# Performance work log

Measured on AMD Instinct MI355X. Metric: run time of the kernel, lower is better.

Reference implementation:

```python
import jax, jax.numpy as jnp
import numpy as np
import math

B, N, D, SEQ = 4, 1024, 512, 256
HID, DIST_D, N_NER, N_LAB = 150, 128, 3, 4
SPANS_PER_WORD = 0.5
ASPECT, OPINION = 1, 2
NUM_DIST_EMB = 512


def setup_inputs() -> dict:
    key = jax.random.key(0)
    ks = jax.random.split(key, 9)
    starts = jax.random.randint(ks[0], (B, N), 0, SEQ)
    widths = jax.random.randint(ks[1], (B, N), 0, 8)
    ends = jnp.clip(starts + widths, 0, SEQ - 1)
    spans = jnp.stack([starts, ends], axis=-1).astype(jnp.int32)  # [B,N,2]
    ner_scores = jax.random.normal(ks[2], (B, N, N_NER), jnp.float32)
    span_embeddings = jax.random.normal(ks[3], (B, N, D), jnp.float32)
    span_mask = jnp.ones((B, N), dtype=bool)

    pair_dim = 2 * D + DIST_D

    def xavier(k, shape):
        std = math.sqrt(2.0 / (shape[0] + shape[1]))
        return jax.random.normal(k, shape, jnp.float32) * std

    dist_table = xavier(ks[4], (NUM_DIST_EMB, DIST_D))
    W1 = xavier(ks[5], (pair_dim, HID)); b1 = jnp.zeros((HID,), jnp.float32)
    W2 = xavier(ks[6], (HID, HID));      b2 = jnp.zeros((HID,), jnp.float32)
    Wc = xavier(ks[7], (HID, N_LAB));    bc = jnp.zeros((N_LAB,), jnp.float32)

    return dict(spans=spans, ner_scores=ner_scores, span_embeddings=span_embeddings,
                span_mask=span_mask, seq_length=SEQ, dist_table=dist_table,
                W1=W1, b1=b1, W2=W2, b2=b2, Wc=Wc, bc=bc)


def bucket_values(d, num_identity=4, num_total=10):
    # semi-logscale buckets: [0,1,2,3,4,5-7,8-15,16-31,32-63,64+]
    logspace = jnp.floor(jnp.log2(jnp.maximum(d, 1).astype(jnp.float32))).astype(jnp.int32) + (num_identity - 1)
    return jnp.clip(jnp.where(d <= num_identity, d, logspace), 0, num_total - 1)


def _prune(scores, mask, k):
    masked = jnp.where(mask, scores, jnp.float32(-1e20))
    _, idx = jax.lax.top_k(masked, k)  # [B,k]
    return idx


def reference(spans, ner_scores, span_embeddings, span_mask, seq_length,
              dist_table, W1, b1, W2, b2, Wc, bc):
    bsz, n_spans, d = span_embeddings.shape
    k = min(int(math.ceil(seq_length * SPANS_PER_WORD)), n_spans)

    a_idx = _prune(ner_scores[..., ASPECT], span_mask, k)    # [B,k]
    o_idx = _prune(ner_scores[..., OPINION], span_mask, k)
    a_keep = jnp.ones((bsz, k), dtype=bool)  # uniform seq_length -> all kept
    o_keep = a_keep

    gather = lambda t, i: jnp.take_along_axis(t, i[..., None], axis=1)
    a_emb = gather(span_embeddings, a_idx)   # [B,k,D]
    o_emb = gather(span_embeddings, o_idx)   # [B,k,D]
    spans_a = gather(spans, a_idx)           # [B,k,2]
    spans_o = gather(spans, o_idx)           # [B,k,2]

    # pairwise min span distance -> bucket -> embedding
    dis1 = jnp.abs(spans_a[..., 0][:, :, None] - spans_o[..., 1][:, None, :])
    dis2 = jnp.abs(spans_a[..., 1][:, :, None] - spans_o[..., 0][:, None, :])
    dis = jnp.minimum(dis1, dis2)                      # [B,k,k]
    dist_emb = dist_table[bucket_values(dis)]          # [B,k,k,DIST_D]

    pair = jnp.concatenate([
        jnp.broadcast_to(a_emb[:, :, None, :], (bsz, k, k, d)),
        jnp.broadcast_to(o_emb[:, None, :, :], (bsz, k, k, d)),
        dist_emb,
    ], axis=-1)                                        # [B,k,k,2D+DIST_D]

    # FeedForward (2 layers, ReLU, dropout=identity at eval) + classifier
    h = jax.nn.relu(pair @ W1 + b1)
    h = jax.nn.relu(h @ W2 + b2)
    scores = h @ Wc + bc                               # [B,k,k,n_labels]

    rel_mask = a_keep[:, :, None] & o_keep[:, None, :]
    return (jax.nn.softmax(scores, axis=-1), rel_mask, pair, spans_a, spans_o)
```

## Files before the change

kernel.cpp:

```cpp
#include <hip/hip_runtime.h>
#include <hip/hip_bf16.h>

#define BB 4
#define NN 1024
#define DD 512
#define KK 128
#define HID 150
#define HIDP 160
#define W2TS 176
#define DIST_D 128
#define PAIRD 1152

typedef __attribute__((ext_vector_type(4))) float f32x4;
typedef __attribute__((ext_vector_type(8))) short s16x8;

__device__ __forceinline__ int bucket_of(int dd) {
    return (dd <= 4) ? dd : min(34 - __clz(dd), 9);
}

__global__ __launch_bounds__(1024) void k_topk(const int* __restrict__ spans,
                                               const float* __restrict__ ner,
                                               const float* __restrict__ dist_table,
                                               const float* __restrict__ W1,
                                               const float* __restrict__ b1,
                                               const float* __restrict__ W2,
                                               int* ws_aidx, int* ws_oidx,
                                               int* ws_sa, int* ws_so,
                                               float* ws_cd, __hip_bfloat16* ws_w2t,
                                               float* out3, float* out4) {
    int t = threadIdx.x;
    int bx = blockIdx.x;
    if (bx < 8) {
        __shared__ unsigned long long sk[NN];
        int b = bx >> 1;
        int which = bx & 1;
        int ch = which ? 2 : 1;
        float v = ner[(b * NN + t) * 3 + ch];
        unsigned int u = __float_as_uint(v);
        unsigned int s = (u & 0x80000000u) ? ~u : (u ^ 0x80000000u);
        unsigned long long mine = ((unsigned long long)s << 32) | (unsigned int)(NN - 1 - t);
        sk[t] = mine;
        __syncthreads();
        int cnt = 0;
#pragma unroll 16
        for (int d = 0; d < NN; ++d) cnt += (sk[d] > mine) ? 1 : 0;
        if (cnt < KK) {
            int idx = t;
            int s0 = spans[(b * NN + idx) * 2];
            int s1 = spans[(b * NN + idx) * 2 + 1];
            int row = b * KK + cnt;
            if (which == 0) {
                ws_aidx[row] = idx;
                ws_sa[row * 2] = s0; ws_sa[row * 2 + 1] = s1;
                out3[row * 2] = (float)s0; out3[row * 2 + 1] = (float)s1;
            } else {
                ws_oidx[row] = idx;
                ws_so[row * 2] = s0; ws_so[row * 2 + 1] = s1;
                out4[row * 2] = (float)s0; out4[row * 2 + 1] = (float)s1;
            }
        }
    } else if (bx < 18) {
        int bk = bx - 8;
        if (t < HIDP) {
            float acc = 0.f;
            if (t < HID) {
                acc = b1[t];
                for (int d = 0; d < DIST_D; ++d)
                    acc = fmaf(dist_table[bk * DIST_D + d], W1[(size_t)(2 * DD + d) * HID + t], acc);
            }
            ws_cd[bk * HIDP + t] = acc;
        }
    } else {
        int e = (bx - 18) * 1024 + t;
        if (e < HIDP * W2TS) {
            int n = e / W2TS, d = e - n * W2TS;
            float v = (n < HID && d < HID) ? W2[d * HID + n] : 0.f;
            ws_w2t[e] = __float2bfloat16(v);
        }
    }
}

__global__ __launch_bounds__(256) void k_contrib(const float* __restrict__ emb,
                                                 const float* __restrict__ W1,
                                                 const int* __restrict__ ws_aidx,
                                                 const int* __restrict__ ws_oidx,
                                                 float* ws_ca, float* ws_co) {
    __shared__ __align__(16) float es[4][DD];
    int t = threadIdx.x;
    int bx = blockIdx.x;
    int which = bx >> 7;
    int row0 = (bx & 127) * 4;
    const int* idxsrc = which ? ws_oidx : ws_aidx;
    for (int x = t; x < 512; x += 256) {
        int r = x >> 7, c = x & 127;
        int row = row0 + r;
        int b = row >> 7;
        int idx = idxsrc[row];
        ((float4*)es[r])[c] = ((const float4*)(emb + ((size_t)(b * NN) + idx) * DD))[c];
    }
    __syncthreads();
    if (t < HIDP) {
        float a0 = 0.f, a1 = 0.f, a2 = 0.f, a3 = 0.f;
        if (t < HID) {
            const float* w = W1 + (size_t)(which * DD) * HID + t;
#pragma unroll 4
            for (int d4 = 0; d4 < 128; ++d4) {
                float4 e0 = ((const float4*)es[0])[d4];
                float4 e1 = ((const float4*)es[1])[d4];
                float4 e2 = ((const float4*)es[2])[d4];
                float4 e3 = ((const float4*)es[3])[d4];
                float w0 = w[(size_t)(4 * d4 + 0) * HID];
                float w1v = w[(size_t)(4 * d4 + 1) * HID];
                float w2v = w[(size_t)(4 * d4 + 2) * HID];
                float w3 = w[(size_t)(4 * d4 + 3) * HID];
                a0 = fmaf(e0.x, w0, a0); a0 = fmaf(e0.y, w1v, a0); a0 = fmaf(e0.z, w2v, a0); a0 = fmaf(e0.w, w3, a0);
                a1 = fmaf(e1.x, w0, a1); a1 = fmaf(e1.y, w1v, a1); a1 = fmaf(e1.z, w2v, a1); a1 = fmaf(e1.w, w3, a1);
                a2 = fmaf(e2.x, w0, a2); a2 = fmaf(e2.y, w1v, a2); a2 = fmaf(e2.z, w2v, a2); a2 = fmaf(e2.w, w3, a2);
                a3 = fmaf(e3.x, w0, a3); a3 = fmaf(e3.y, w1v, a3); a3 = fmaf(e3.z, w2v, a3); a3 = fmaf(e3.w, w3, a3);
            }
        }
        float* dstb = which ? ws_co : ws_ca;
        dstb[(row0 + 0) * HIDP + t] = a0;
        dstb[(row0 + 1) * HIDP + t] = a1;
        dstb[(row0 + 2) * HIDP + t] = a2;
        dstb[(row0 + 3) * HIDP + t] = a3;
    }
}

__global__ __launch_bounds__(256, 2) void k_fused(const float* __restrict__ emb,
                                                  const float* __restrict__ dist_table,
                                                  const float* __restrict__ Wc,
                                                  const float* __restrict__ bcp,
                                                  const float* __restrict__ b2p,
                                                  const int* __restrict__ ws_aidx,
                                                  const int* __restrict__ ws_oidx,
                                                  const int* __restrict__ ws_sa,
                                                  const int* __restrict__ ws_so,
                                                  const float* __restrict__ ws_ca,
                                                  const float* __restrict__ ws_co,
                                                  const float* __restrict__ ws_cd,
                                                  const __hip_bfloat16* __restrict__ ws_w2t,
                                                  float* __restrict__ out0,
                                                  float* __restrict__ out1,
                                                  float* __restrict__ out2) {
    int t = threadIdx.x;
    int bx = blockIdx.x;

    if (bx >= 4608) {
        int i = (bx - 4608) * 256 + t;
        ((float4*)out1)[i] = make_float4(1.f, 1.f, 1.f, 1.f);
        return;
    }

    if (bx % 9 == 0) {
        int bi = bx / 9;
        int b = bi >> 7;
        int wave = t >> 6, l = t & 63;
        int lc = l & 15, lg = l >> 4;
        int r0 = wave * 32 + lc, r1 = r0 + 16;

        int sa0 = ws_sa[bi * 2], sa1 = ws_sa[bi * 2 + 1];
        int so00 = ws_so[(b * KK + r0) * 2], so01 = ws_so[(b * KK + r0) * 2 + 1];
        int so10 = ws_so[(b * KK + r1) * 2], so11 = ws_so[(b * KK + r1) * 2 + 1];
        int bkt0 = bucket_of(min(abs(sa0 - so01), abs(sa1 - so00)));
        int bkt1 = bucket_of(min(abs(sa0 - so11), abs(sa1 - so10)));

        const f32x4* ca4 = (const f32x4*)(ws_ca + (size_t)bi * HIDP);
        const f32x4* co04 = (const f32x4*)(ws_co + (size_t)(b * KK + r0) * HIDP);
        const f32x4* co14 = (const f32x4*)(ws_co + (size_t)(b * KK + r1) * HIDP);
        const f32x4* cd04 = (const f32x4*)(ws_cd + (size_t)bkt0 * HIDP);
        const f32x4* cd14 = (const f32x4*)(ws_cd + (size_t)bkt1 * HIDP);

        s16x8 af0[5], af1[5];
        union U8 { s16x8 frag; __hip_bfloat16 h[8]; };
#pragma unroll
        for (int kk = 0; kk < 5; ++kk) {
            int o = kk * 8 + lg * 2;
            f32x4 caa = ca4[o], cab = ca4[o + 1];
            f32x4 s0a = caa + co04[o] + cd04[o];
            f32x4 s0b = cab + co04[o + 1] + cd04[o + 1];
            f32x4 s1a = caa + co14[o] + cd14[o];
            f32x4 s1b = cab + co14[o + 1] + cd14[o + 1];
            U8 u0, u1;
#pragma unroll
            for (int e = 0; e < 4; ++e) {
                u0.h[e]     = __float2bfloat16(fmaxf(s0a[e], 0.f));
                u0.h[e + 4] = __float2bfloat16(fmaxf(s0b[e], 0.f));
                u1.h[e]     = __float2bfloat16(fmaxf(s1a[e], 0.f));
                u1.h[e + 4] = __float2bfloat16(fmaxf(s1b[e], 0.f));
            }
            af0[kk] = u0.frag;
            af1[kk] = u1.frag;
        }

        f32x4 acc[2][10];
#pragma unroll
        for (int mi = 0; mi < 2; ++mi)
#pragma unroll
            for (int nt = 0; nt < 10; ++nt)
                acc[mi][nt] = (f32x4){0.f, 0.f, 0.f, 0.f};

#pragma unroll
        for (int kk = 0; kk < 5; ++kk) {
#pragma unroll
            for (int nt = 0; nt < 10; ++nt) {
                s16x8 bf = *(const s16x8*)&ws_w2t[(nt * 16 + lc) * W2TS + kk * 32 + lg * 8];
                acc[0][nt] = __builtin_amdgcn_mfma_f32_16x16x32_bf16(af0[kk], bf, acc[0][nt], 0, 0, 0);
                acc[1][nt] = __builtin_amdgcn_mfma_f32_16x16x32_bf16(af1[kk], bf, acc[1][nt], 0, 0, 0);
            }
        }

        float4 wcv[10];
        float b2v[10];
#pragma unroll
        for (int nt = 0; nt < 10; ++nt) {
            int n = nt * 16 + lc;
            if (n < HID) {
                wcv[nt] = *(const float4*)(Wc + n * 4);
                b2v[nt] = b2p[n];
            } else {
                wcv[nt] = make_float4(0.f, 0.f, 0.f, 0.f);
                b2v[nt] = 0.f;
            }
        }
        float bc0 = bcp[0], bc1 = bcp[1], bc2 = bcp[2], bc3 = bcp[3];

#pragma unroll
        for (int mi = 0; mi < 2; ++mi) {
#pragma unroll
            for (int r = 0; r < 4; ++r) {
                int j = wave * 32 + mi * 16 + lg * 4 + r;
                float p0 = 0.f, p1 = 0.f, p2 = 0.f, p3 = 0.f;
#pragma unroll
                for (int nt = 0; nt < 10; ++nt) {
                    float h2 = fmaxf(acc[mi][nt][r] + b2v[nt], 0.f);
                    p0 = fmaf(h2, wcv[nt].x, p0);
                    p1 = fmaf(h2, wcv[nt].y, p1);
                    p2 = fmaf(h2, wcv[nt].z, p2);
                    p3 = fmaf(h2, wcv[nt].w, p3);
                }
#pragma unroll
                for (int m = 8; m >= 1; m >>= 1) {
                    p0 += __shfl_xor(p0, m, 16);
                    p1 += __shfl_xor(p1, m, 16);
                    p2 += __shfl_xor(p2, m, 16);
                    p3 += __shfl_xor(p3, m, 16);
                }
                p0 += bc0; p1 += bc1; p2 += bc2; p3 += bc3;
                float mx = fmaxf(fmaxf(p0, p1), fmaxf(p2, p3));
                float e0 = expf(p0 - mx), e1 = expf(p1 - mx), e2 = expf(p2 - mx), e3 = expf(p3 - mx);
                float inv = 1.f / (e0 + e1 + e2 + e3);
                if (lc < 4) {
                    float v = (lc == 0) ? e0 : (lc == 1) ? e1 : (lc == 2) ? e2 : e3;
                    out0[((size_t)bi * KK + j) * 4 + lc] = v * inv;
                }
            }
        }
    } else {
        int pid = bx - bx / 9 - 1;
        int bi = pid >> 3, jc = pid & 7;
        int b = bi >> 7;
        int j0 = jc << 4;
        int c = t & 127;
        int half = t >> 7;

        const float4* ebase = (const float4*)(emb + (size_t)b * NN * DD);

        int aidx = ws_aidx[bi];
        float4 areg = ebase[(size_t)aidx * 128 + c];

        float4 oreg[8];
#pragma unroll
        for (int it = 0; it < 8; ++it) {
            int j = it * 2 + half;
            int oidx = ws_oidx[b * KK + j0 + j];
            oreg[it] = ebase[(size_t)oidx * 128 + c];
        }

        int sa0 = ws_sa[bi * 2], sa1 = ws_sa[bi * 2 + 1];
        float4 dreg[2];
        int dj[2], dc[2];
#pragma unroll
        for (int it = 0; it < 2; ++it) {
            int x = it * 256 + t;
            dj[it] = x >> 5; dc[it] = x & 31;
            int so0 = ws_so[(b * KK + j0 + dj[it]) * 2];
            int so1 = ws_so[(b * KK + j0 + dj[it]) * 2 + 1];
            int bkt = bucket_of(min(abs(sa0 - so1), abs(sa1 - so0)));
            dreg[it] = ((const float4*)dist_table)[bkt * 32 + dc[it]];
        }

        float4* dst = (float4*)(out2 + (size_t)bi * (KK * PAIRD)) + (size_t)j0 * 288;
#pragma unroll
        for (int it = 0; it < 8; ++it) {
            int j = it * 2 + half;
            dst[j * 288 + c] = areg;
            dst[j * 288 + 128 + c] = oreg[it];
        }
#pragma unroll
        for (int it = 0; it < 2; ++it) {
            dst[dj[it] * 288 + 256 + dc[it]] = dreg[it];
        }
    }
}

extern "C" void kernel_launch(void* const* d_in, const int* in_sizes, int n_in,
                              void* d_out, int out_size, void* d_ws, size_t ws_size,
                              hipStream_t stream) {
    const int*   spans = (const int*)d_in[0];
    const float* ner   = (const float*)d_in[1];
    const float* emb   = (const float*)d_in[2];
    const float* dist_table = (const float*)d_in[5];
    const float* W1 = (const float*)d_in[6];
    const float* b1 = (const float*)d_in[7];
    const float* W2 = (const float*)d_in[8];
    const float* b2 = (const float*)d_in[9];
    const float* Wc = (const float*)d_in[10];
    const float* bc = (const float*)d_in[11];

    float* out0 = (float*)d_out;
    float* out1 = out0 + (size_t)BB * KK * KK * 4;
    float* out2 = out1 + (size_t)BB * KK * KK;
    float* out3 = out2 + (size_t)BB * KK * KK * PAIRD;
    float* out4 = out3 + (size_t)BB * KK * 2;

    int* ws_aidx = (int*)d_ws;
    int* ws_oidx = ws_aidx + BB * KK;
    int* ws_sa   = ws_oidx + BB * KK;
    int* ws_so   = ws_sa + BB * KK * 2;
    float* ws_ca = (float*)(ws_so + BB * KK * 2);
    float* ws_co = ws_ca + BB * KK * HIDP;
    float* ws_cd = ws_co + BB * KK * HIDP;
    __hip_bfloat16* ws_w2t = (__hip_bfloat16*)(ws_cd + 16 * HIDP);

    k_topk<<<46, 1024, 0, stream>>>(spans, ner, dist_table, W1, b1, W2,
                                    ws_aidx, ws_oidx, ws_sa, ws_so,
                                    ws_cd, ws_w2t, out3, out4);
    k_contrib<<<256, 256, 0, stream>>>(emb, W1, ws_aidx, ws_oidx, ws_ca, ws_co);
    k_fused<<<4672, 256, 0, stream>>>(emb, dist_table, Wc, bc, b2,
                                      ws_aidx, ws_oidx, ws_sa, ws_so,
                                      ws_ca, ws_co, ws_cd, ws_w2t,
                                      out0, out1, out2);
}
```

Baseline: 104.2 us.

## Reorder MFMA loop per output tile to cut accumulator registers, raise occupancy

Swaps the loop order in the second-layer MFMA so each 16-column output tile is fully accumulated over K and then immediately folded into the classifier partial sums, rather than keeping all 20 accumulator vectors live. This shrinks live registers from 80 accumulator floats to 32 partial-sum floats plus two tiles, and the launch bound is raised from 2 to 4 blocks per SIMD to use the freed registers for occupancy. The cost is a serial dependency chain of 5 MFMAs per tile with less interleaving, and W2 loads are now issued per tile inside the loop.

Result: slower. 117.5 us (+12.8%).

```diff
diff --git a/kernel.cpp b/kernel.cpp
--- a/kernel.cpp
+++ b/kernel.cpp
@@ -127,7 +127,7 @@
     }
 }
 
-__global__ __launch_bounds__(256, 2) void k_fused(const float* __restrict__ emb,
+__global__ __launch_bounds__(256, 4) void k_fused(const float* __restrict__ emb,
                                                   const float* __restrict__ dist_table,
                                                   const float* __restrict__ Wc,
                                                   const float* __restrict__ bcp,
@@ -193,52 +193,56 @@
             af1[kk] = u1.frag;
         }
 
-        f32x4 acc[2][10];
+        float p[2][4][4];
 #pragma unroll
         for (int mi = 0; mi < 2; ++mi)
 #pragma unroll
-            for (int nt = 0; nt < 10; ++nt)
-                acc[mi][nt] = (f32x4){0.f, 0.f, 0.f, 0.f};
-
-#pragma unroll
-        for (int kk = 0; kk < 5; ++kk) {
-#pragma unroll
-            for (int nt = 0; nt < 10; ++nt) {
-                s16x8 bf = *(const s16x8*)&ws_w2t[(nt * 16 + lc) * W2TS + kk * 32 + lg * 8];
-                acc[0][nt] = __builtin_amdgcn_mfma_f32_16x16x32_bf16(af0[kk], bf, acc[0][nt], 0, 0, 0);
-                acc[1][nt] = __builtin_amdgcn_mfma_f32_16x16x32_bf16(af1[kk], bf, acc[1][nt], 0, 0, 0);
-            }
-        }
-
-        float4 wcv[10];
-        float b2v[10];
+            for (int r = 0; r < 4; ++r)
+#pragma unroll
+                for (int cls = 0; cls < 4; ++cls) p[mi][r][cls] = 0.f;
+
 #pragma unroll
         for (int nt = 0; nt < 10; ++nt) {
             int n = nt * 16 + lc;
+            f32x4 acc0 = (f32x4){0.f, 0.f, 0.f, 0.f};
+            f32x4 acc1 = (f32x4){0.f, 0.f, 0.f, 0.f};
+#pragma unroll
+            for (int kk = 0; kk < 5; ++kk) {
+                s16x8 bf = *(const s16x8*)&ws_w2t[(nt * 16 + lc) * W2TS + kk * 32 + lg * 8];
+                acc0 = __builtin_amdgcn_mfma_f32_16x16x32_bf16(af0[kk], bf, acc0, 0, 0, 0);
+                acc1 = __builtin_amdgcn_mfma_f32_16x16x32_bf16(af1[kk], bf, acc1, 0, 0, 0);
+            }
+            float4 wc;
+            float b2v;
             if (n < HID) {
-                wcv[nt] = *(const float4*)(Wc + n * 4);
-                b2v[nt] = b2p[n];
+                wc = *(const float4*)(Wc + n * 4);
+                b2v = b2p[n];
             } else {
-                wcv[nt] = make_float4(0.f, 0.f, 0.f, 0.f);
-                b2v[nt] = 0.f;
-            }
-        }
+                wc = make_float4(0.f, 0.f, 0.f, 0.f);
+                b2v = 0.f;
+            }
+#pragma unroll
+            for (int r = 0; r < 4; ++r) {
+                float h20 = fmaxf(acc0[r] + b2v, 0.f);
+                float h21 = fmaxf(acc1[r] + b2v, 0.f);
+                p[0][r][0] = fmaf(h20, wc.x, p[0][r][0]);
+                p[0][r][1] = fmaf(h20, wc.y, p[0][r][1]);
+                p[0][r][2] = fmaf(h20, wc.z, p[0][r][2]);
+                p[0][r][3] = fmaf(h20, wc.w, p[0][r][3]);
+                p[1][r][0] = fmaf(h21, wc.x, p[1][r][0]);
+                p[1][r][1] = fmaf(h21, wc.y, p[1][r][1]);
+                p[1][r][2] = fmaf(h21, wc.z, p[1][r][2]);
+                p[1][r][3] = fmaf(h21, wc.w, p[1][r][3]);
+            }
+        }
+
         float bc0 = bcp[0], bc1 = bcp[1], bc2 = bcp[2], bc3 = bcp[3];
-
 #pragma unroll
         for (int mi = 0; mi < 2; ++mi) {
 #pragma unroll
             for (int r = 0; r < 4; ++r) {
                 int j = wave * 32 + mi * 16 + lg * 4 + r;
-                float p0 = 0.f, p1 = 0.f, p2 = 0.f, p3 = 0.f;
-#pragma unroll
-                for (int nt = 0; nt < 10; ++nt) {
-                    float h2 = fmaxf(acc[mi][nt][r] + b2v[nt], 0.f);
-                    p0 = fmaf(h2, wcv[nt].x, p0);
-                    p1 = fmaf(h2, wcv[nt].y, p1);
-                    p2 = fmaf(h2, wcv[nt].z, p2);
-                    p3 = fmaf(h2, wcv[nt].w, p3);
-                }
+                float p0 = p[mi][r][0], p1 = p[mi][r][1], p2 = p[mi][r][2], p3 = p[mi][r][3];
 #pragma unroll
                 for (int m = 8; m >= 1; m >>= 1) {
                     p0 += __shfl_xor(p0, m, 16);
```
